# Performance work log

Hardware: AMD Instinct MI355X
Metric: run time of the kernel (lower is better)

The kernel has to match this reference:

```python
import jax, jax.numpy as jnp
import numpy as np

B, N, K, D = 64, 1024, 512, 256  # batch, positions, codes, H*W


def setup_inputs() -> dict:
    key = jax.random.key(0)
    k1, k2 = jax.random.split(key)
    z_e_x = jax.random.normal(k1, (B, N, D), dtype=jnp.float32)
    # nn.Embedding(K, H*W) initialized uniform(-1/K, 1/K)
    codebook = jax.random.uniform(k2, (K, D), dtype=jnp.float32,
                                  minval=-1.0 / K, maxval=1.0 / K)
    return {"z_e_x": z_e_x, "codebook": codebook}


def _nearest_code(flat, codebook):
    # squared L2 distance via expansion: ||z||^2 - 2 z.e + ||e||^2
    d = ((flat * flat).sum(-1, keepdims=True)
         - 2.0 * flat @ codebook.T
         + (codebook * codebook).sum(-1))  # [M, K]
    return jnp.argmin(d, axis=-1)  # [M]


def reference(z_e_x, codebook):
    # Faithful to VQEmbedding.straight_through(z_e_x):
    #   z_q_x: quantized with straight-through estimator (grad -> z_e_x)
    #   z_q_x_bar: gather from live codebook (grad -> codebook)
    flat = z_e_x.reshape(-1, codebook.shape[1])  # [M, D]
    idx = _nearest_code(flat, jax.lax.stop_gradient(codebook))
    cb_sg = jax.lax.stop_gradient(codebook)
    z_q_st = flat + jax.lax.stop_gradient(cb_sg[idx] - flat)
    z_q_x = z_q_st.reshape(z_e_x.shape)
    z_q_x_bar = codebook[idx].reshape(z_e_x.shape)
    return z_q_x, z_q_x_bar
```

## Files before the change

### kernel.cpp

```cpp
#include <hip/hip_runtime.h>
#include <math.h>
#include <limits.h>

#define M_ROWS 65536
#define DD     256
#define KC     512
#define TILE_M 128
#define CHUNK  128
#define KS     32

__device__ __forceinline__ float pw128_sq(const float4* __restrict__ q) {
  float r[8];
  {
    float4 a = q[0], b = q[1];
    r[0] = __fmul_rn(a.x, a.x); r[1] = __fmul_rn(a.y, a.y);
    r[2] = __fmul_rn(a.z, a.z); r[3] = __fmul_rn(a.w, a.w);
    r[4] = __fmul_rn(b.x, b.x); r[5] = __fmul_rn(b.y, b.y);
    r[6] = __fmul_rn(b.z, b.z); r[7] = __fmul_rn(b.w, b.w);
  }
#pragma unroll
  for (int i = 2; i < 32; i += 2) {
    float4 a = q[i], b = q[i + 1];
    r[0] = __fadd_rn(r[0], __fmul_rn(a.x, a.x));
    r[1] = __fadd_rn(r[1], __fmul_rn(a.y, a.y));
    r[2] = __fadd_rn(r[2], __fmul_rn(a.z, a.z));
    r[3] = __fadd_rn(r[3], __fmul_rn(a.w, a.w));
    r[4] = __fadd_rn(r[4], __fmul_rn(b.x, b.x));
    r[5] = __fadd_rn(r[5], __fmul_rn(b.y, b.y));
    r[6] = __fadd_rn(r[6], __fmul_rn(b.z, b.z));
    r[7] = __fadd_rn(r[7], __fmul_rn(b.w, b.w));
  }
  return __fadd_rn(__fadd_rn(__fadd_rn(r[0], r[1]), __fadd_rn(r[2], r[3])),
                   __fadd_rn(__fadd_rn(r[4], r[5]), __fadd_rn(r[6], r[7])));
}

__global__ void sumsq_kernel(const float* __restrict__ x, float* __restrict__ s,
                             int nrows) {
  int r = blockIdx.x * blockDim.x + threadIdx.x;
  if (r >= nrows) return;
  const float4* q = (const float4*)(x + (size_t)r * DD);
  s[r] = __fadd_rn(pw128_sq(q), pw128_sq(q + 32));
}

__global__ __launch_bounds__(256) void vq_kernel(
    const float* __restrict__ z, const float* __restrict__ cb,
    const float* __restrict__ s, const float* __restrict__ se,
    float* __restrict__ out) {
  __shared__ float4 zs4[TILE_M * 8];
  __shared__ float4 es4[CHUNK * 8];
  __shared__ float s_l[TILE_M];
  __shared__ float se_l[KC];
  __shared__ int   best_l[TILE_M];

  const int tid = threadIdx.x;
  const int tx = tid & 15, ty = tid >> 4;
  const int txs = tx & 7, tys = ty & 7;
  const int r0 = blockIdx.x * TILE_M;

  if (tid < TILE_M) s_l[tid] = s[r0 + tid];
  se_l[tid] = se[tid];
  se_l[tid + 256] = se[tid + 256];

  float bestd[8];
  int   besti[8];
#pragma unroll
  for (int i = 0; i < 8; ++i) { bestd[i] = INFINITY; besti[i] = INT_MAX; }

  const float4* zg = (const float4*)z;
  const float4* cg = (const float4*)cb;

  for (int ch = 0; ch < KC / CHUNK; ++ch) {
    const int cbase = ch * CHUNK;
    float acc[8][8];
#pragma unroll
    for (int i = 0; i < 8; ++i)
#pragma unroll
      for (int j = 0; j < 8; ++j) acc[i][j] = 0.0f;

    for (int ks = 0; ks < DD / KS; ++ks) {
      __syncthreads();
#pragma unroll
      for (int p = 0; p < 4; ++p) {
        int u = p * 256 + tid;
        int row = u >> 3, q = u & 7;
        zs4[(row << 3) | (q ^ ((row >> 3) & 7))] =
            zg[(size_t)(r0 + row) * 64 + ks * 8 + q];
      }
#pragma unroll
      for (int p = 0; p < 4; ++p) {
        int u = p * 256 + tid;
        int crow = u >> 3, q = u & 7;
        es4[(crow << 3) | (q ^ ((crow >> 3) & 7))] =
            cg[(size_t)(cbase + crow) * 64 + ks * 8 + q];
      }
      __syncthreads();

#pragma unroll
      for (int k4 = 0; k4 < 8; ++k4) {
        const int kz = k4 ^ tys;
        const int ke = k4 ^ txs;
        float4 zf[8];
#pragma unroll
        for (int i = 0; i < 8; ++i) zf[i] = zs4[((ty * 8 + i) << 3) | kz];
#pragma unroll
        for (int j = 0; j < 8; ++j) {
          float4 ef = es4[((tx * 8 + j) << 3) | ke];
#pragma unroll
          for (int i = 0; i < 8; ++i) {
            acc[i][j] = __fmaf_rn(zf[i].x, ef.x, acc[i][j]);
            acc[i][j] = __fmaf_rn(zf[i].y, ef.y, acc[i][j]);
            acc[i][j] = __fmaf_rn(zf[i].z, ef.z, acc[i][j]);
            acc[i][j] = __fmaf_rn(zf[i].w, ef.w, acc[i][j]);
          }
        }
      }
    }

#pragma unroll
    for (int i = 0; i < 8; ++i) {
      float s_r = s_l[ty * 8 + i];
#pragma unroll
      for (int j = 0; j < 8; ++j) {
        int code = cbase + tx * 8 + j;
        float d = __fadd_rn(__fsub_rn(s_r, __fmul_rn(2.0f, acc[i][j])),
                            se_l[code]);
        if (d < bestd[i] || (d == bestd[i] && code < besti[i])) {
          bestd[i] = d; besti[i] = code;
        }
      }
    }
  }

#pragma unroll
  for (int i = 0; i < 8; ++i) {
    float bd = bestd[i];
    int   bi = besti[i];
#pragma unroll
    for (int off = 1; off < 16; off <<= 1) {
      float od = __shfl_xor(bd, off, 64);
      int   oi = __shfl_xor(bi, off, 64);
      if (od < bd || (od == bd && oi < bi)) { bd = od; bi = oi; }
    }
    if (tx == 0) best_l[ty * 8 + i] = bi;
  }
  __syncthreads();

  float4* out0 = (float4*)out;
  float4* out1 = (float4*)(out + (size_t)M_ROWS * DD);
#pragma unroll
  for (int it = 0; it < (TILE_M * 64) / 256; ++it) {
    int u = it * 256 + tid;
    int row = u >> 6, c4 = u & 63;
    size_t gidx = (size_t)(r0 + row) * 64 + c4;
    float4 zv = zg[gidx];
    float4 cv = cg[(size_t)best_l[row] * 64 + c4];
    float4 o0;
    o0.x = __fadd_rn(zv.x, __fsub_rn(cv.x, zv.x));
    o0.y = __fadd_rn(zv.y, __fsub_rn(cv.y, zv.y));
    o0.z = __fadd_rn(zv.z, __fsub_rn(cv.z, zv.z));
    o0.w = __fadd_rn(zv.w, __fsub_rn(cv.w, zv.w));
    out0[gidx] = o0;
    out1[gidx] = cv;
  }
}

extern "C" void kernel_launch(void* const* d_in, const int* in_sizes, int n_in,
                              void* d_out, int out_size, void* d_ws, size_t ws_size,
                              hipStream_t stream) {
  const float* z  = (const float*)d_in[0];
  const float* cb = (const float*)d_in[1];
  float* out = (float*)d_out;
  float* s  = (float*)d_ws;
  float* se = s + M_ROWS;

  sumsq_kernel<<<M_ROWS / 256, 256, 0, stream>>>(z, s, M_ROWS);
  sumsq_kernel<<<KC / 256, 256, 0, stream>>>(cb, se, KC);
  vq_kernel<<<M_ROWS / TILE_M, 256, 0, stream>>>(z, cb, s, se, out);
}
```

Baseline: 274.7 us.

## Split codebook chunks across blocks and combine argmin in a separate kernel

```diff
diff --git a/kernel.cpp b/kernel.cpp
--- a/kernel.cpp
+++ b/kernel.cpp
@@ -7,6 +7,7 @@
 #define KC     512
 #define TILE_M 128
 #define CHUNK  128
+#define NCH    (KC / CHUNK)
 #define KS     32
 
 __device__ __forceinline__ float pw128_sq(const float4* __restrict__ q) {
@@ -42,24 +43,26 @@
   s[r] = __fadd_rn(pw128_sq(q), pw128_sq(q + 32));
 }
 
-__global__ __launch_bounds__(256) void vq_kernel(
+__global__ __launch_bounds__(256) void vq_partial_kernel(
     const float* __restrict__ z, const float* __restrict__ cb,
     const float* __restrict__ s, const float* __restrict__ se,
-    float* __restrict__ out) {
+    float* __restrict__ pd, int* __restrict__ pi) {
   __shared__ float4 zs4[TILE_M * 8];
   __shared__ float4 es4[CHUNK * 8];
   __shared__ float s_l[TILE_M];
-  __shared__ float se_l[KC];
-  __shared__ int   best_l[TILE_M];
+  __shared__ float se_l[CHUNK];
 
   const int tid = threadIdx.x;
   const int tx = tid & 15, ty = tid >> 4;
   const int txs = tx & 7, tys = ty & 7;
-  const int r0 = blockIdx.x * TILE_M;
+  const int bid = blockIdx.x;
+  const int mt = bid >> 2;
+  const int ch = bid & 3;
+  const int r0 = mt * TILE_M;
+  const int cbase = ch * CHUNK;
 
   if (tid < TILE_M) s_l[tid] = s[r0 + tid];
-  se_l[tid] = se[tid];
-  se_l[tid + 256] = se[tid + 256];
+  if (tid < CHUNK) se_l[tid] = se[cbase + tid];
 
   float bestd[8];
   int   besti[8];
@@ -69,64 +72,61 @@
   const float4* zg = (const float4*)z;
   const float4* cg = (const float4*)cb;
 
-  for (int ch = 0; ch < KC / CHUNK; ++ch) {
-    const int cbase = ch * CHUNK;
-    float acc[8][8];
-#pragma unroll
-    for (int i = 0; i < 8; ++i)
-#pragma unroll
-      for (int j = 0; j < 8; ++j) acc[i][j] = 0.0f;
-
-    for (int ks = 0; ks < DD / KS; ++ks) {
-      __syncthreads();
-#pragma unroll
-      for (int p = 0; p < 4; ++p) {
-        int u = p * 256 + tid;
-        int row = u >> 3, q = u & 7;
-        zs4[(row << 3) | (q ^ ((row >> 3) & 7))] =
-            zg[(size_t)(r0 + row) * 64 + ks * 8 + q];
-      }
-#pragma unroll
-      for (int p = 0; p < 4; ++p) {
-        int u = p * 256 + tid;
-        int crow = u >> 3, q = u & 7;
-        es4[(crow << 3) | (q ^ ((crow >> 3) & 7))] =
-            cg[(size_t)(cbase + crow) * 64 + ks * 8 + q];
-      }
-      __syncthreads();
-
-#pragma unroll
-      for (int k4 = 0; k4 < 8; ++k4) {
-        const int kz = k4 ^ tys;
-        const int ke = k4 ^ txs;
-        float4 zf[8];
-#pragma unroll
-        for (int i = 0; i < 8; ++i) zf[i] = zs4[((ty * 8 + i) << 3) | kz];
-#pragma unroll
-        for (int j = 0; j < 8; ++j) {
-          float4 ef = es4[((tx * 8 + j) << 3) | ke];
-#pragma unroll
-          for (int i = 0; i < 8; ++i) {
-            acc[i][j] = __fmaf_rn(zf[i].x, ef.x, acc[i][j]);
-            acc[i][j] = __fmaf_rn(zf[i].y, ef.y, acc[i][j]);
-            acc[i][j] = __fmaf_rn(zf[i].z, ef.z, acc[i][j]);
-            acc[i][j] = __fmaf_rn(zf[i].w, ef.w, acc[i][j]);
-          }
+  float acc[8][8];
+#pragma unroll
+  for (int i = 0; i < 8; ++i)
+#pragma unroll
+    for (int j = 0; j < 8; ++j) acc[i][j] = 0.0f;
+
+  for (int ks = 0; ks < DD / KS; ++ks) {
+    __syncthreads();
+#pragma unroll
+    for (int p = 0; p < 4; ++p) {
+      int u = p * 256 + tid;
+      int row = u >> 3, q = u & 7;
+      zs4[(row << 3) | (q ^ ((row >> 3) & 7))] =
+          zg[(size_t)(r0 + row) * 64 + ks * 8 + q];
+    }
+#pragma unroll
+    for (int p = 0; p < 4; ++p) {
+      int u = p * 256 + tid;
+      int crow = u >> 3, q = u & 7;
+      es4[(crow << 3) | (q ^ ((crow >> 3) & 7))] =
+          cg[(size_t)(cbase + crow) * 64 + ks * 8 + q];
+    }
+    __syncthreads();
+
+#pragma unroll
+    for (int k4 = 0; k4 < 8; ++k4) {
+      const int kz = k4 ^ tys;
+      const int ke = k4 ^ txs;
+      float4 zf[8];
+#pragma unroll
+      for (int i = 0; i < 8; ++i) zf[i] = zs4[((ty * 8 + i) << 3) | kz];
+#pragma unroll
+      for (int j = 0; j < 8; ++j) {
+        float4 ef = es4[((tx * 8 + j) << 3) | ke];
+#pragma unroll
+        for (int i = 0; i < 8; ++i) {
+          acc[i][j] = __fmaf_rn(zf[i].x, ef.x, acc[i][j]);
+          acc[i][j] = __fmaf_rn(zf[i].y, ef.y, acc[i][j]);
+          acc[i][j] = __fmaf_rn(zf[i].z, ef.z, acc[i][j]);
+          acc[i][j] = __fmaf_rn(zf[i].w, ef.w, acc[i][j]);
         }
       }
     }
-
-#pragma unroll
-    for (int i = 0; i < 8; ++i) {
-      float s_r = s_l[ty * 8 + i];
-#pragma unroll
-      for (int j = 0; j < 8; ++j) {
-        int code = cbase + tx * 8 + j;
-        float d = __fadd_rn(__fsub_rn(s_r, __fmul_rn(2.0f, acc[i][j])),
-                            se_l[code]);
-        if (d < bestd[i] || (d == bestd[i] && code < besti[i])) {
-          bestd[i] = d; besti[i] = code;
-        }
+  }
+
+#pragma unroll
+  for (int i = 0; i < 8; ++i) {
+    float s_r = s_l[ty * 8 + i];
+#pragma unroll
+    for (int j = 0; j < 8; ++j) {
+      int code = cbase + tx * 8 + j;
+      float d = __fadd_rn(__fsub_rn(s_r, __fmul_rn(2.0f, acc[i][j])),
+                          se_l[code - cbase]);
+      if (d < bestd[i] || (d == bestd[i] && code < besti[i])) {
+        bestd[i] = d; besti[i] = code;
       }
     }
   }
@@ -141,14 +141,42 @@
       int   oi = __shfl_xor(bi, off, 64);
       if (od < bd || (od == bd && oi < bi)) { bd = od; bi = oi; }
     }
-    if (tx == 0) best_l[ty * 8 + i] = bi;
+    if (tx == 0) {
+      int row = r0 + ty * 8 + i;
+      pd[(size_t)ch * M_ROWS + row] = bd;
+      pi[(size_t)ch * M_ROWS + row] = bi;
+    }
+  }
+}
+
+__global__ __launch_bounds__(256) void combine_kernel(
+    const float* __restrict__ z, const float* __restrict__ cb,
+    const float* __restrict__ pd, const int* __restrict__ pi,
+    float* __restrict__ out) {
+  __shared__ int best_l[128];
+  const int tid = threadIdx.x;
+  const int r0 = blockIdx.x * 128;
+
+  if (tid < 128) {
+    int row = r0 + tid;
+    float bd = INFINITY;
+    int   bi = INT_MAX;
+#pragma unroll
+    for (int c = 0; c < NCH; ++c) {
+      float d = pd[(size_t)c * M_ROWS + row];
+      int   i2 = pi[(size_t)c * M_ROWS + row];
+      if (d < bd || (d == bd && i2 < bi)) { bd = d; bi = i2; }
+    }
+    best_l[tid] = bi;
   }
   __syncthreads();
 
+  const float4* zg = (const float4*)z;
+  const float4* cg = (const float4*)cb;
   float4* out0 = (float4*)out;
   float4* out1 = (float4*)(out + (size_t)M_ROWS * DD);
 #pragma unroll
-  for (int it = 0; it < (TILE_M * 64) / 256; ++it) {
+  for (int it = 0; it < (128 * 64) / 256; ++it) {
     int u = it * 256 + tid;
     int row = u >> 6, c4 = u & 63;
     size_t gidx = (size_t)(r0 + row) * 64 + c4;
@@ -172,8 +200,11 @@
   float* out = (float*)d_out;
   float* s  = (float*)d_ws;
   float* se = s + M_ROWS;
+  float* pd = se + KC;
+  int*   pi = (int*)(pd + (size_t)NCH * M_ROWS);
 
   sumsq_kernel<<<M_ROWS / 256, 256, 0, stream>>>(z, s, M_ROWS);
   sumsq_kernel<<<KC / 256, 256, 0, stream>>>(cb, se, KC);
-  vq_kernel<<<M_ROWS / TILE_M, 256, 0, stream>>>(z, cb, s, se, out);
-}
+  vq_partial_kernel<<<(M_ROWS / TILE_M) * NCH, 256, 0, stream>>>(z, cb, s, se, pd, pi);
+  combine_kernel<<<M_ROWS / 128, 256, 0, stream>>>(z, cb, pd, pi, out);
+}
```

Measured after the change: 284.0 us. 3.4% more time.

## Double-buffer LDS tiles using direct global-to-LDS async loads

Applied to the files above, without the earlier changes.

```diff
diff --git a/kernel.cpp b/kernel.cpp
--- a/kernel.cpp
+++ b/kernel.cpp
@@ -42,88 +42,117 @@
   s[r] = __fadd_rn(pw128_sq(q), pw128_sq(q + 32));
 }
 
+typedef __attribute__((address_space(1))) const void gas_void;
+typedef __attribute__((address_space(3))) void las_void;
+__device__ __forceinline__ void gl_lds16(const void* g, void* l) {
+  __builtin_amdgcn_global_load_lds((gas_void*)g, (las_void*)l, 16, 0, 0);
+}
+
 __global__ __launch_bounds__(256) void vq_kernel(
     const float* __restrict__ z, const float* __restrict__ cb,
     const float* __restrict__ s, const float* __restrict__ se,
     float* __restrict__ out) {
-  __shared__ float4 zs4[TILE_M * 8];
-  __shared__ float4 es4[CHUNK * 8];
-  __shared__ float s_l[TILE_M];
-  __shared__ float se_l[KC];
-  __shared__ int   best_l[TILE_M];
+  __shared__ float4 zs4[2][TILE_M * 8];
+  __shared__ float4 es4[2][CHUNK * 8];
 
   const int tid = threadIdx.x;
   const int tx = tid & 15, ty = tid >> 4;
   const int txs = tx & 7, tys = ty & 7;
+  const int wv = tid >> 6;
+  const int lane = tid & 63;
   const int r0 = blockIdx.x * TILE_M;
 
-  if (tid < TILE_M) s_l[tid] = s[r0 + tid];
-  se_l[tid] = se[tid];
-  se_l[tid + 256] = se[tid + 256];
+  const float4* zg = (const float4*)z;
+  const float4* cg = (const float4*)cb;
+
+  float s_reg[8];
+#pragma unroll
+  for (int i = 0; i < 8; ++i) s_reg[i] = s[r0 + ty * 8 + i];
 
   float bestd[8];
   int   besti[8];
 #pragma unroll
   for (int i = 0; i < 8; ++i) { bestd[i] = INFINITY; besti[i] = INT_MAX; }
 
-  const float4* zg = (const float4*)z;
-  const float4* cg = (const float4*)cb;
-
+  auto stage_z = [&](int b, int ks) {
+#pragma unroll
+    for (int seg = 0; seg < 4; ++seg) {
+      int u = (wv * 4 + seg) * 64 + lane;
+      int row = u >> 3, qs = u & 7;
+      int q = qs ^ ((row >> 3) & 7);
+      gl_lds16(&zg[(size_t)(r0 + row) * 64 + ks * 8 + q],
+               (char*)&zs4[b][0] + (wv * 4 + seg) * 1024);
+    }
+  };
+  auto stage_e = [&](int b, int cbase, int ks) {
+#pragma unroll
+    for (int seg = 0; seg < 4; ++seg) {
+      int u = (wv * 4 + seg) * 64 + lane;
+      int row = u >> 3, qs = u & 7;
+      int q = qs ^ ((row >> 3) & 7);
+      gl_lds16(&cg[(size_t)(cbase + row) * 64 + ks * 8 + q],
+               (char*)&es4[b][0] + (wv * 4 + seg) * 1024);
+    }
+  };
+
+  auto compute = [&](int b, float (&acc)[8][8]) {
+#pragma unroll
+    for (int k4 = 0; k4 < 8; ++k4) {
+      const float4* zp = &zs4[b][ty * 64 + (k4 ^ tys)];
+      const float4* ep = &es4[b][tx * 64 + (k4 ^ txs)];
+      float4 zf[8];
+#pragma unroll
+      for (int i = 0; i < 8; ++i) zf[i] = zp[i * 8];
+#pragma unroll
+      for (int j = 0; j < 8; ++j) {
+        float4 ef = ep[j * 8];
+#pragma unroll
+        for (int i = 0; i < 8; ++i) {
+          acc[i][j] = __fmaf_rn(zf[i].x, ef.x, acc[i][j]);
+          acc[i][j] = __fmaf_rn(zf[i].y, ef.y, acc[i][j]);
+          acc[i][j] = __fmaf_rn(zf[i].z, ef.z, acc[i][j]);
+          acc[i][j] = __fmaf_rn(zf[i].w, ef.w, acc[i][j]);
+        }
+      }
+    }
+  };
+
+#pragma unroll 1
   for (int ch = 0; ch < KC / CHUNK; ++ch) {
     const int cbase = ch * CHUNK;
+    float se_reg[8];
+#pragma unroll
+    for (int j = 0; j < 8; ++j) se_reg[j] = se[cbase + tx * 8 + j];
+
     float acc[8][8];
 #pragma unroll
     for (int i = 0; i < 8; ++i)
 #pragma unroll
       for (int j = 0; j < 8; ++j) acc[i][j] = 0.0f;
 
+    stage_z(0, 0);
+    stage_e(0, cbase, 0);
+    __syncthreads();
+
+    int b = 0;
+#pragma unroll 1
     for (int ks = 0; ks < DD / KS; ++ks) {
+      if (ks < DD / KS - 1) {
+        stage_z(b ^ 1, ks + 1);
+        stage_e(b ^ 1, cbase, ks + 1);
+      }
+      compute(b, acc);
       __syncthreads();
-#pragma unroll
-      for (int p = 0; p < 4; ++p) {
-        int u = p * 256 + tid;
-        int row = u >> 3, q = u & 7;
-        zs4[(row << 3) | (q ^ ((row >> 3) & 7))] =
-            zg[(size_t)(r0 + row) * 64 + ks * 8 + q];
-      }
-#pragma unroll
-      for (int p = 0; p < 4; ++p) {
-        int u = p * 256 + tid;
-        int crow = u >> 3, q = u & 7;
-        es4[(crow << 3) | (q ^ ((crow >> 3) & 7))] =
-            cg[(size_t)(cbase + crow) * 64 + ks * 8 + q];
-      }
-      __syncthreads();
-
-#pragma unroll
-      for (int k4 = 0; k4 < 8; ++k4) {
-        const int kz = k4 ^ tys;
-        const int ke = k4 ^ txs;
-        float4 zf[8];
-#pragma unroll
-        for (int i = 0; i < 8; ++i) zf[i] = zs4[((ty * 8 + i) << 3) | kz];
-#pragma unroll
-        for (int j = 0; j < 8; ++j) {
-          float4 ef = es4[((tx * 8 + j) << 3) | ke];
-#pragma unroll
-          for (int i = 0; i < 8; ++i) {
-            acc[i][j] = __fmaf_rn(zf[i].x, ef.x, acc[i][j]);
-            acc[i][j] = __fmaf_rn(zf[i].y, ef.y, acc[i][j]);
-            acc[i][j] = __fmaf_rn(zf[i].z, ef.z, acc[i][j]);
-            acc[i][j] = __fmaf_rn(zf[i].w, ef.w, acc[i][j]);
-          }
-        }
-      }
+      b ^= 1;
     }
 
 #pragma unroll
     for (int i = 0; i < 8; ++i) {
-      float s_r = s_l[ty * 8 + i];
 #pragma unroll
       for (int j = 0; j < 8; ++j) {
         int code = cbase + tx * 8 + j;
-        float d = __fadd_rn(__fsub_rn(s_r, __fmul_rn(2.0f, acc[i][j])),
-                            se_l[code]);
+        float d = __fadd_rn(__fsub_rn(s_reg[i], __fmul_rn(2.0f, acc[i][j])),
+                            se_reg[j]);
         if (d < bestd[i] || (d == bestd[i] && code < besti[i])) {
           bestd[i] = d; besti[i] = code;
         }
@@ -131,6 +160,7 @@
     }
   }
 
+  int* best_l = (int*)&zs4[0][0];
 #pragma unroll
   for (int i = 0; i < 8; ++i) {
     float bd = bestd[i];
```

Result: slower. 377.2 us (+37.3%).

## Replace LDS-tiled GEMM with per-wave register tiling and direct global loads

Applied to the files above, without the earlier changes.

```diff
diff --git a/kernel.cpp b/kernel.cpp
--- a/kernel.cpp
+++ b/kernel.cpp
@@ -5,9 +5,6 @@
 #define M_ROWS 65536
 #define DD     256
 #define KC     512
-#define TILE_M 128
-#define CHUNK  128
-#define KS     32
 
 __device__ __forceinline__ float pw128_sq(const float4* __restrict__ q) {
   float r[8];
@@ -46,111 +43,97 @@
     const float* __restrict__ z, const float* __restrict__ cb,
     const float* __restrict__ s, const float* __restrict__ se,
     float* __restrict__ out) {
-  __shared__ float4 zs4[TILE_M * 8];
-  __shared__ float4 es4[CHUNK * 8];
-  __shared__ float s_l[TILE_M];
-  __shared__ float se_l[KC];
-  __shared__ int   best_l[TILE_M];
+  __shared__ int best_l[32];
 
   const int tid = threadIdx.x;
-  const int tx = tid & 15, ty = tid >> 4;
-  const int txs = tx & 7, tys = ty & 7;
-  const int r0 = blockIdx.x * TILE_M;
+  const int lane = tid & 63;
+  const int wv = tid >> 6;
+  const int rowbase =
+      __builtin_amdgcn_readfirstlane((int)blockIdx.x * 32 + wv * 8);
 
-  if (tid < TILE_M) s_l[tid] = s[r0 + tid];
-  se_l[tid] = se[tid];
-  se_l[tid + 256] = se[tid + 256];
+  const float4* zq = (const float4*)(z + (size_t)rowbase * DD);
+  const float4* cq = (const float4*)(cb + (size_t)(lane * 8) * DD);
 
-  float bestd[8];
-  int   besti[8];
+  float se_reg[8];
+  {
+    const float4* sq = (const float4*)(se + lane * 8);
+    float4 a = sq[0], b = sq[1];
+    se_reg[0] = a.x; se_reg[1] = a.y; se_reg[2] = a.z; se_reg[3] = a.w;
+    se_reg[4] = b.x; se_reg[5] = b.y; se_reg[6] = b.z; se_reg[7] = b.w;
+  }
+
+  float acc[8][8];
 #pragma unroll
-  for (int i = 0; i < 8; ++i) { bestd[i] = INFINITY; besti[i] = INT_MAX; }
+  for (int i = 0; i < 8; ++i)
+#pragma unroll
+    for (int j = 0; j < 8; ++j) acc[i][j] = 0.0f;
 
-  const float4* zg = (const float4*)z;
-  const float4* cg = (const float4*)cb;
+  float4 efa[8], efb[8];
+#pragma unroll
+  for (int j = 0; j < 8; ++j) efa[j] = cq[j * 64];
 
-  for (int ch = 0; ch < KC / CHUNK; ++ch) {
-    const int cbase = ch * CHUNK;
-    float acc[8][8];
+#pragma unroll 1
+  for (int k4 = 0; k4 < 64; k4 += 2) {
 #pragma unroll
-    for (int i = 0; i < 8; ++i)
+    for (int j = 0; j < 8; ++j) efb[j] = cq[j * 64 + k4 + 1];
 #pragma unroll
-      for (int j = 0; j < 8; ++j) acc[i][j] = 0.0f;
-
-    for (int ks = 0; ks < DD / KS; ++ks) {
-      __syncthreads();
+    for (int i = 0; i < 8; ++i) {
+      float4 zf = zq[i * 64 + k4];
 #pragma unroll
-      for (int p = 0; p < 4; ++p) {
-        int u = p * 256 + tid;
-        int row = u >> 3, q = u & 7;
-        zs4[(row << 3) | (q ^ ((row >> 3) & 7))] =
-            zg[(size_t)(r0 + row) * 64 + ks * 8 + q];
-      }
-#pragma unroll
-      for (int p = 0; p < 4; ++p) {
-        int u = p * 256 + tid;
-        int crow = u >> 3, q = u & 7;
-        es4[(crow << 3) | (q ^ ((crow >> 3) & 7))] =
-            cg[(size_t)(cbase + crow) * 64 + ks * 8 + q];
-      }
-      __syncthreads();
-
-#pragma unroll
-      for (int k4 = 0; k4 < 8; ++k4) {
-        const int kz = k4 ^ tys;
-        const int ke = k4 ^ txs;
-        float4 zf[8];
-#pragma unroll
-        for (int i = 0; i < 8; ++i) zf[i] = zs4[((ty * 8 + i) << 3) | kz];
-#pragma unroll
-        for (int j = 0; j < 8; ++j) {
-          float4 ef = es4[((tx * 8 + j) << 3) | ke];
-#pragma unroll
-          for (int i = 0; i < 8; ++i) {
-            acc[i][j] = __fmaf_rn(zf[i].x, ef.x, acc[i][j]);
-            acc[i][j] = __fmaf_rn(zf[i].y, ef.y, acc[i][j]);
-            acc[i][j] = __fmaf_rn(zf[i].z, ef.z, acc[i][j]);
-            acc[i][j] = __fmaf_rn(zf[i].w, ef.w, acc[i][j]);
-          }
-        }
+      for (int j = 0; j < 8; ++j) {
+        acc[i][j] = __fmaf_rn(zf.x, efa[j].x, acc[i][j]);
+        acc[i][j] = __fmaf_rn(zf.y, efa[j].y, acc[i][j]);
+        acc[i][j] = __fmaf_rn(zf.z, efa[j].z, acc[i][j]);
+        acc[i][j] = __fmaf_rn(zf.w, efa[j].w, acc[i][j]);
       }
     }
-
+    const int nk4 = (k4 + 2 < 64) ? (k4 + 2) : 0;
+#pragma unroll
+    for (int j = 0; j < 8; ++j) efa[j] = cq[j * 64 + nk4];
 #pragma unroll
     for (int i = 0; i < 8; ++i) {
-      float s_r = s_l[ty * 8 + i];
+      float4 zf = zq[i * 64 + k4 + 1];
 #pragma unroll
       for (int j = 0; j < 8; ++j) {
-        int code = cbase + tx * 8 + j;
-        float d = __fadd_rn(__fsub_rn(s_r, __fmul_rn(2.0f, acc[i][j])),
-                            se_l[code]);
-        if (d < bestd[i] || (d == bestd[i] && code < besti[i])) {
-          bestd[i] = d; besti[i] = code;
-        }
+        acc[i][j] = __fmaf_rn(zf.x, efb[j].x, acc[i][j]);
+        acc[i][j] = __fmaf_rn(zf.y, efb[j].y, acc[i][j]);
+        acc[i][j] = __fmaf_rn(zf.z, efb[j].z, acc[i][j]);
+        acc[i][j] = __fmaf_rn(zf.w, efb[j].w, acc[i][j]);
       }
     }
   }
 
 #pragma unroll
   for (int i = 0; i < 8; ++i) {
-    float bd = bestd[i];
-    int   bi = besti[i];
+    float s_r = s[rowbase + i];
+    float bd = INFINITY;
+    int   bi = INT_MAX;
 #pragma unroll
-    for (int off = 1; off < 16; off <<= 1) {
+    for (int j = 0; j < 8; ++j) {
+      int code = lane * 8 + j;
+      float d = __fadd_rn(__fsub_rn(s_r, __fmul_rn(2.0f, acc[i][j])),
+                          se_reg[j]);
+      if (d < bd || (d == bd && code < bi)) { bd = d; bi = code; }
+    }
+#pragma unroll
+    for (int off = 1; off < 64; off <<= 1) {
       float od = __shfl_xor(bd, off, 64);
       int   oi = __shfl_xor(bi, off, 64);
       if (od < bd || (od == bd && oi < bi)) { bd = od; bi = oi; }
     }
-    if (tx == 0) best_l[ty * 8 + i] = bi;
+    if (lane == 0) best_l[wv * 8 + i] = bi;
   }
   __syncthreads();
 
+  const int r0 = blockIdx.x * 32;
+  const float4* zg = (const float4*)z;
+  const float4* cg = (const float4*)cb;
   float4* out0 = (float4*)out;
   float4* out1 = (float4*)(out + (size_t)M_ROWS * DD);
 #pragma unroll
-  for (int it = 0; it < (TILE_M * 64) / 256; ++it) {
-    int u = it * 256 + tid;
-    int row = u >> 6, c4 = u & 63;
+  for (int it = 0; it < 8; ++it) {
+    int row = it * 4 + wv;
+    int c4 = lane;
     size_t gidx = (size_t)(r0 + row) * 64 + c4;
     float4 zv = zg[gidx];
     float4 cv = cg[(size_t)best_l[row] * 64 + c4];
@@ -175,5 +158,5 @@
 
   sumsq_kernel<<<M_ROWS / 256, 256, 0, stream>>>(z, s, M_ROWS);
   sumsq_kernel<<<KC / 256, 256, 0, stream>>>(cb, se, KC);
-  vq_kernel<<<M_ROWS / TILE_M, 256, 0, stream>>>(z, cb, s, se, out);
+  vq_kernel<<<M_ROWS / 32, 256, 0, stream>>>(z, cb, s, se, out);
 }
```

Measured after the change: 765.8 us. 2.79x slower.
